# Kernel optimization log

Measured on AMD Instinct MI355X. Metric: run time of the kernel, lower is better.

Reference implementation:

```python
import jax, jax.numpy as jnp
import numpy as np
from jax.scipy.special import digamma, gammaln

B, N, H, W, D = 16, 1024, 32, 32, 256
TEMP = 0.5
KL_WEIGHT = 1e-3


def setup_inputs() -> dict:
    key = jax.random.key(0)
    k1, k2, k3 = jax.random.split(key, 3)
    logits = jax.random.normal(k1, (B, N, H, W), dtype=jnp.float32)
    # codebook initialized uniform(-1/N, 1/N) as in init_type == 'uniform'
    codebook = jax.random.uniform(k2, (N, D), dtype=jnp.float32,
                                  minval=-1.0 / N, maxval=1.0 / N)
    # uniform noise for the Gumbel-softmax rsample (channels-last layout [B,H,W,N])
    uniform_noise = jax.random.uniform(k3, (B, H, W, N), dtype=jnp.float32,
                                       minval=1e-6, maxval=1.0 - 1e-6)
    return {"logits": logits, "codebook": codebook, "uniform_noise": uniform_noise}


def reference(logits, codebook, uniform_noise):
    # convert_to_alpha: evidential mapping alpha = softplus(logits) + 1,
    # then permute(0,2,3,1) -> [B, H, W, N]
    alpha = jax.nn.softplus(jnp.transpose(logits, (0, 2, 3, 1))) + 1.0
    S = jnp.sum(alpha, axis=-1, keepdims=True)            # [B,H,W,1]
    probs = alpha / S                                      # [B,H,W,N]

    # RelaxedOneHotCategorical(temp, probs).rsample() == Gumbel-softmax
    gumbel = -jnp.log(-jnp.log(uniform_noise))
    sample = jax.nn.softmax((jnp.log(probs) + gumbel) / TEMP, axis=-1)  # [B,H,W,N]

    vector_weights = jnp.transpose(sample, (0, 3, 1, 2))   # [B,N,H,W]
    indices = jnp.argmax(vector_weights, axis=1)           # [B,H,W]

    # quantized output via codebook combine
    z_q = jnp.einsum('bnhw,nd->bdhw', vector_weights, codebook)  # [B,D,H,W]

    # KL( Dirichlet(alpha) || Dirichlet(ones(N)) ), closed form with beta=1:
    # lgamma(S) - sum lgamma(alpha) - lgamma(N) + sum (alpha-1)*(digamma(alpha)-digamma(S))
    S1 = S[..., 0]
    kl = (gammaln(S1)
          - jnp.sum(gammaln(alpha), axis=-1)
          - gammaln(jnp.float32(N))
          + jnp.sum((alpha - 1.0) * (digamma(alpha) - digamma(S)), axis=-1))
    kl_loss = KL_WEIGHT * jnp.mean(kl)

    # perplexity over soft encodings
    avg_probs = jnp.mean(sample.reshape(-1, N), axis=0)
    perplexity = jnp.exp(-jnp.sum(avg_probs * jnp.log(avg_probs + 1e-10)))

    return (z_q, kl_loss, indices, perplexity)
```

## Files before the change

### kernel.cpp

```cpp
#include <hip/hip_runtime.h>
#include <math.h>

#define NB 16
#define NN 1024
#define NH 32
#define NW 32
#define ND 256
#define NPIX (NB*NH*NW)

#define ZQ_OFF  0
#define KL_OFF  4194304
#define IDX_OFF 4194305
#define PPL_OFF 4210689

#define LGAMMA_1024F 6071.2804f
#define BS_ROW_B 2080

typedef _Float16 f16x8 __attribute__((ext_vector_type(8)));
typedef _Float16 f16x4 __attribute__((ext_vector_type(4)));
typedef float    f32x4 __attribute__((ext_vector_type(4)));

__device__ __forceinline__ float fast_rcp(float x){ return __builtin_amdgcn_rcpf(x); }

__device__ __forceinline__ void lgamma_digamma(float a, float& lg, float& dg){
    float a1 = a + 1.f, a2 = a + 2.f, a3 = a + 3.f, z = a + 4.f;
    float p01 = a*a1, p23 = a2*a3;
    float prod = p01*p23;
    float rz = fast_rcp(z);
    float rp = fast_rcp(prod);
    float lz = __logf(z);
    float lp = __logf(prod);
    float rz2 = rz*rz;
    lg = (z - 0.5f)*lz - z + 0.918938533f
       + rz*(0.083333333f - 0.002777778f*rz2) - lp;
    float sr = ((a + a + 1.f)*p23 + (a + a + 5.f)*p01)*rp;
    dg = lz - 0.5f*rz - rz2*(0.083333333f - 0.008333333f*rz2) - sr;
}

__device__ __forceinline__ float elem(float x, float u,
                                      float& S, float& L, float& P){
    float t  = __expf(-fabsf(x));
    float a  = fmaxf(x, 0.f) + __logf(1.f + t) + 1.f;
    float lg, dg;
    lgamma_digamma(a, lg, dg);
    S += a; L += lg; P += (a - 1.f)*dg;
    float d = 1.f - u;
    float lup = -d*(1.f + d*(0.5f + d*(0.33333333f + d*(0.25f
              + d*(0.2f + d*(0.16666667f + d*0.14285714f))))));
    float lu = (d < 0.09f) ? lup : __logf(u);
    float ar = a * fast_rcp(lu);
    return ar*ar;
}

__global__ __launch_bounds__(256) void k_tr(
    const float* __restrict__ cb, _Float16* __restrict__ cbT)
{
    const int kb = blockIdx.x, kq = blockIdx.y, d = threadIdx.x;
    _Float16 tmp[8];
#pragma unroll
    for (int i = 0; i < 8; ++i)
        tmp[i] = (_Float16)cb[(size_t)(32*kb + 8*kq + i)*ND + d];
    *(f16x8*)(cbT + (size_t)kb*8192 + (size_t)d*32 + 8*kq) = *(f16x8*)tmp;
}

__global__ __launch_bounds__(512, 4) void k_mega(
    const float* __restrict__ logits, const float* __restrict__ noise,
    const _Float16* __restrict__ cbT, float* __restrict__ colpart,
    float* __restrict__ klpart, float* __restrict__ out)
{
    __shared__ __align__(16) char lds[16*BS_ROW_B + 6*128*4];
    char*  bsb  = lds;
    float* redS = (float*)(lds + 16*BS_ROW_B);
    float* redL = redS + 128;
    float* redP = redL + 128;
    float* redZ = redP + 128;
    float* redM = redZ + 128;
    int*   redI = (int*)(redM + 128);

    const int t    = threadIdx.x;
    const int row  = blockIdx.x >> 1;
    const int w0   = (blockIdx.x & 1) * 16;
    const int b    = row >> 5, h = row & 31;
    const int lane = t & 63;
    const int v    = t >> 6;
    const int wl   = lane & 15;
    const int j4   = lane >> 4;
    const int p    = row*32 + w0 + wl;
    const int nq   = 4*v + j4;

    const float* lgB = logits + (size_t)b*(NN*NH*NW) + (size_t)(4*nq)*(NH*NW)
                     + (size_t)h*NW + w0 + wl;
    const float* nzB = noise  + (size_t)p*NN + 4*nq;

    float4 u4[8];
    float  xs[8][4];
    float  ev[32];
    float S = 0.f, L = 0.f, P = 0.f, Z = 0.f;
    float mx = -1.f;
    int   idx = 0;

#define CHUNK_LOAD(kk) do{                                        \
    u4[kk] = *(const float4*)(nzB + 128*(kk));                    \
    xs[kk][0] = lgB[(size_t)(128*(kk)+0)*(NH*NW)];                \
    xs[kk][1] = lgB[(size_t)(128*(kk)+1)*(NH*NW)];                \
    xs[kk][2] = lgB[(size_t)(128*(kk)+2)*(NH*NW)];                \
    xs[kk][3] = lgB[(size_t)(128*(kk)+3)*(NH*NW)]; }while(0)

#define DO_E(kk,mm,UC) do{                                        \
    float e = elem(xs[kk][mm], UC, S, L, P);                      \
    Z += e;                                                       \
    if (e > mx){ mx = e; idx = 128*(kk) + 4*nq + (mm); }          \
    ev[4*(kk)+(mm)] = e; }while(0)

    CHUNK_LOAD(0); CHUNK_LOAD(1); CHUNK_LOAD(2);
#pragma unroll
    for (int k = 0; k < 8; ++k){
        if (k < 5) CHUNK_LOAD(k+3);
        DO_E(k,0,u4[k].x);
        DO_E(k,1,u4[k].y);
        DO_E(k,2,u4[k].z);
        DO_E(k,3,u4[k].w);
    }
#undef CHUNK_LOAD
#undef DO_E

#pragma unroll
    for (int mask = 16; mask < 64; mask <<= 1){
        S += __shfl_xor(S, mask);
        L += __shfl_xor(L, mask);
        P += __shfl_xor(P, mask);
        Z += __shfl_xor(Z, mask);
        float mo = __shfl_xor(mx, mask);
        int   io = __shfl_xor(idx, mask);
        bool take = (mo > mx) || (mo == mx && io < idx);
        mx  = take ? mo : mx;
        idx = take ? io : idx;
    }
    if (j4 == 0){
        redS[16*v + wl] = S;  redL[16*v + wl] = L;
        redP[16*v + wl] = P;  redZ[16*v + wl] = Z;
        redM[16*v + wl] = mx; redI[16*v + wl] = idx;
    }
    __syncthreads();

    float Zt = 0.f;
#pragma unroll
    for (int qz = 0; qz < 8; ++qz) Zt += redZ[16*qz + wl];
    const float zinv = fast_rcp(Zt);

    {
        char* brow = bsb + wl*BS_ROW_B;
        const int sw   = wl & 7;
        const int sub8 = (nq & 1) << 3;
        const int cb2  = nq >> 1;
#pragma unroll
        for (int k = 0; k < 8; ++k){
            f16x4 hv;
            hv[0] = (_Float16)(ev[4*k+0]*zinv);
            hv[1] = (_Float16)(ev[4*k+1]*zinv);
            hv[2] = (_Float16)(ev[4*k+2]*zinv);
            hv[3] = (_Float16)(ev[4*k+3]*zinv);
            *(f16x4*)(brow + (((16*k + cb2) ^ sw) << 4) + sub8) = hv;
        }
    }

    if (t < 16){
        float Sa = 0.f, La = 0.f, Pa = 0.f, M = -1.f;
        int I = 0x7fffffff;
#pragma unroll
        for (int qz = 0; qz < 8; ++qz){
            Sa += redS[16*qz + t]; La += redL[16*qz + t]; Pa += redP[16*qz + t];
            float m = redM[16*qz + t]; int i = redI[16*qz + t];
            bool take = (m > M) || (m == M && i < I);
            M = take ? m : M; I = take ? i : I;
        }
        out[IDX_OFF + row*32 + w0 + t] = (float)I;
        float rS  = fast_rcp(Sa);
        float lnS = __logf(Sa);
        float lgS = (Sa - 0.5f)*lnS - Sa + 0.918938533f + 0.083333333f*rS;
        float dgS = lnS - 0.5f*rS;
        float kl = lgS - La - LGAMMA_1024F + (Pa - dgS*(Sa - 1024.f));
#pragma unroll
        for (int mask = 1; mask < 16; mask <<= 1) kl += __shfl_xor(kl, mask);
        if (t == 0) klpart[blockIdx.x] = kl;
    }
    __syncthreads();

    const _Float16* aBase = cbT + (size_t)(32*v + wl)*32 + j4*8;
    const char* bRow = bsb + wl*BS_ROW_B;
    const int fsw = wl & 7;

    f32x4 acc0 = (f32x4)0.f, acc1 = (f32x4)0.f;
    f16x8 a0[3], a1[3];
    a0[0] = *(const f16x8*)(aBase);
    a1[0] = *(const f16x8*)(aBase + 512);
    a0[1] = *(const f16x8*)(aBase + 8192);
    a1[1] = *(const f16x8*)(aBase + 8192 + 512);

#pragma unroll
    for (int kb = 0; kb < 32; ++kb){
        if (kb + 2 < 32){
            a0[(kb+2)%3] = *(const f16x8*)(aBase + (size_t)(kb+2)*8192);
            a1[(kb+2)%3] = *(const f16x8*)(aBase + (size_t)(kb+2)*8192 + 512);
        }
        f16x8 bf = *(const f16x8*)(bRow + ((((kb << 2) | j4) ^ fsw) << 4));
        acc0 = __builtin_amdgcn_mfma_f32_16x16x32_f16(a0[kb%3], bf, acc0, 0, 0, 0);
        acc1 = __builtin_amdgcn_mfma_f32_16x16x32_f16(a1[kb%3], bf, acc1, 0, 0, 0);
    }

    float* outp = out + (size_t)b*(ND*1024) + h*32 + w0;
#pragma unroll
    for (int r = 0; r < 4; ++r){
        int d = 32*v + 4*j4 + r;
        outp[(size_t)d*1024 + wl]        = acc0[r];
        outp[(size_t)(d + 16)*1024 + wl] = acc1[r];
    }

    {
        float s0 = 0.f, s1 = 0.f;
        const int c0 = t, c1 = t + 512;
#pragma unroll
        for (int r = 0; r < 16; ++r){
            const char* br = bsb + r*BS_ROW_B;
            const int sw2 = r & 7;
            s0 += (float)*(const _Float16*)(br + ((((c0 >> 3) ^ sw2) << 4) + 2*(c0 & 7)));
            s1 += (float)*(const _Float16*)(br + ((((c1 >> 3) ^ sw2) << 4) + 2*(c1 & 7)));
        }
        float* cp = colpart + (size_t)blockIdx.x*NN;
        cp[c0] = s0;
        cp[c1] = s1;
    }
}

__global__ __launch_bounds__(256) void k_red(
    const float* __restrict__ colpart, float* __restrict__ colsum)
{
    __shared__ float red[8][32];
    const int nl = threadIdx.x & 31;
    const int rs = threadIdx.x >> 5;
    const int n  = blockIdx.x*32 + nl;
    const float* cp = colpart + (size_t)rs*128*NN + n;
    float s = 0.f;
#pragma unroll 8
    for (int r = 0; r < 128; ++r)
        s += cp[(size_t)r*NN];
    red[rs][nl] = s;
    __syncthreads();
    if (threadIdx.x < 32){
        float tot = 0.f;
#pragma unroll
        for (int i = 0; i < 8; ++i) tot += red[i][threadIdx.x];
        colsum[blockIdx.x*32 + threadIdx.x] = tot;
    }
}

__global__ __launch_bounds__(256) void k_final(
    const float* __restrict__ colsum, const float* __restrict__ klpart,
    float* __restrict__ out)
{
    __shared__ float red[8];
    const int tid = threadIdx.x;
    float s = 0.f, kls = 0.f;
#pragma unroll
    for (int n = tid; n < NN; n += 256){
        float avg = colsum[n] * (1.f/16384.f);
        s += avg * logf(avg + 1e-10f);
        kls += klpart[n];
    }
#pragma unroll
    for (int mask = 1; mask < 64; mask <<= 1){
        s   += __shfl_xor(s, mask);
        kls += __shfl_xor(kls, mask);
    }
    if ((tid & 63) == 0){ red[tid >> 6] = s; red[4 + (tid >> 6)] = kls; }
    __syncthreads();
    if (tid == 0){
        float tot = red[0] + red[1] + red[2] + red[3];
        float klt = red[4] + red[5] + red[6] + red[7];
        out[PPL_OFF] = expf(-tot);
        out[KL_OFF]  = 1e-3f * (klt * (1.f/16384.f));
    }
}

extern "C" void kernel_launch(void* const* d_in, const int* in_sizes, int n_in,
                              void* d_out, int out_size, void* d_ws, size_t ws_size,
                              hipStream_t stream)
{
    const float* logits = (const float*)d_in[0];
    const float* cb     = (const float*)d_in[1];
    const float* noise  = (const float*)d_in[2];
    float* out = (float*)d_out;

    float* colpart = (float*)d_ws;
    float* colsum  = colpart + (size_t)1024*NN;
    float* klpart  = colsum + NN;
    _Float16* cbT  = (_Float16*)(klpart + NN);

    k_tr   <<<dim3(32, 4), 256, 0, stream>>>(cb, cbT);
    k_mega <<<dim3(1024),  512, 0, stream>>>(logits, noise, cbT, colpart, klpart, out);
    k_red  <<<dim3(32),    256, 0, stream>>>(colpart, colsum);
    k_final<<<1, 256, 0, stream>>>(colsum, klpart, out);
}
```

Baseline: 211.7 us.

## Double block to 1024 threads, halve per-thread work, shorten lgamma shift

The fused kernel now runs 1024 threads per block, so each thread processes 16 codebook entries instead of 32 and each wave computes one 16-wide MFMA output tile instead of two. The intent is more latency hiding and lower register pressure per thread. The lgamma/digamma recurrence shift drops from 4 to 3 terms, which saves arithmetic but may lose some accuracy for small alpha. Scheduling barriers pin the load prefetch order, and the KL reduction is moved after the matmul.

```diff
diff --git a/kernel.cpp b/kernel.cpp
--- a/kernel.cpp
+++ b/kernel.cpp
@@ -23,9 +23,9 @@
 __device__ __forceinline__ float fast_rcp(float x){ return __builtin_amdgcn_rcpf(x); }
 
 __device__ __forceinline__ void lgamma_digamma(float a, float& lg, float& dg){
-    float a1 = a + 1.f, a2 = a + 2.f, a3 = a + 3.f, z = a + 4.f;
-    float p01 = a*a1, p23 = a2*a3;
-    float prod = p01*p23;
+    float a1 = a + 1.f, a2 = a + 2.f, z = a + 3.f;
+    float t12  = a1*a2;
+    float prod = a*t12;
     float rz = fast_rcp(z);
     float rp = fast_rcp(prod);
     float lz = __logf(z);
@@ -33,7 +33,7 @@
     float rz2 = rz*rz;
     lg = (z - 0.5f)*lz - z + 0.918938533f
        + rz*(0.083333333f - 0.002777778f*rz2) - lp;
-    float sr = ((a + a + 1.f)*p23 + (a + a + 5.f)*p01)*rp;
+    float sr = (t12 + a*(a + a + 3.f))*rp;
     dg = lz - 0.5f*rz - rz2*(0.083333333f - 0.008333333f*rz2) - sr;
 }
 
@@ -63,19 +63,19 @@
     *(f16x8*)(cbT + (size_t)kb*8192 + (size_t)d*32 + 8*kq) = *(f16x8*)tmp;
 }
 
-__global__ __launch_bounds__(512, 4) void k_mega(
+__global__ __launch_bounds__(1024, 4) void k_mega(
     const float* __restrict__ logits, const float* __restrict__ noise,
     const _Float16* __restrict__ cbT, float* __restrict__ colpart,
     float* __restrict__ klpart, float* __restrict__ out)
 {
-    __shared__ __align__(16) char lds[16*BS_ROW_B + 6*128*4];
+    __shared__ __align__(16) char lds[16*BS_ROW_B + 6*256*4];
     char*  bsb  = lds;
     float* redS = (float*)(lds + 16*BS_ROW_B);
-    float* redL = redS + 128;
-    float* redP = redL + 128;
-    float* redZ = redP + 128;
-    float* redM = redZ + 128;
-    int*   redI = (int*)(redM + 128);
+    float* redL = redS + 256;
+    float* redP = redL + 256;
+    float* redZ = redP + 256;
+    float* redM = redZ + 256;
+    int*   redI = (int*)(redM + 256);
 
     const int t    = threadIdx.x;
     const int row  = blockIdx.x >> 1;
@@ -84,7 +84,7 @@
     const int lane = t & 63;
     const int v    = t >> 6;
     const int wl   = lane & 15;
-    const int j4   = lane >> 4;
+    const int j4   = (lane >> 4) & 3;
     const int p    = row*32 + w0 + wl;
     const int nq   = 4*v + j4;
 
@@ -92,30 +92,31 @@
                      + (size_t)h*NW + w0 + wl;
     const float* nzB = noise  + (size_t)p*NN + 4*nq;
 
-    float4 u4[8];
-    float  xs[8][4];
-    float  ev[32];
+    float4 u4[4];
+    float  xs[4][4];
+    float  ev[16];
     float S = 0.f, L = 0.f, P = 0.f, Z = 0.f;
     float mx = -1.f;
     int   idx = 0;
 
 #define CHUNK_LOAD(kk) do{                                        \
-    u4[kk] = *(const float4*)(nzB + 128*(kk));                    \
-    xs[kk][0] = lgB[(size_t)(128*(kk)+0)*(NH*NW)];                \
-    xs[kk][1] = lgB[(size_t)(128*(kk)+1)*(NH*NW)];                \
-    xs[kk][2] = lgB[(size_t)(128*(kk)+2)*(NH*NW)];                \
-    xs[kk][3] = lgB[(size_t)(128*(kk)+3)*(NH*NW)]; }while(0)
+    u4[kk] = *(const float4*)(nzB + 256*(kk));                    \
+    xs[kk][0] = lgB[(size_t)(256*(kk)+0)*(NH*NW)];                \
+    xs[kk][1] = lgB[(size_t)(256*(kk)+1)*(NH*NW)];                \
+    xs[kk][2] = lgB[(size_t)(256*(kk)+2)*(NH*NW)];                \
+    xs[kk][3] = lgB[(size_t)(256*(kk)+3)*(NH*NW)]; }while(0)
 
 #define DO_E(kk,mm,UC) do{                                        \
     float e = elem(xs[kk][mm], UC, S, L, P);                      \
     Z += e;                                                       \
-    if (e > mx){ mx = e; idx = 128*(kk) + 4*nq + (mm); }          \
+    if (e > mx){ mx = e; idx = 256*(kk) + 4*nq + (mm); }          \
     ev[4*(kk)+(mm)] = e; }while(0)
 
-    CHUNK_LOAD(0); CHUNK_LOAD(1); CHUNK_LOAD(2);
-#pragma unroll
-    for (int k = 0; k < 8; ++k){
-        if (k < 5) CHUNK_LOAD(k+3);
+    CHUNK_LOAD(0); CHUNK_LOAD(1);
+    __builtin_amdgcn_sched_barrier(0);
+#pragma unroll
+    for (int k = 0; k < 4; ++k){
+        if (k < 2){ CHUNK_LOAD(k+2); __builtin_amdgcn_sched_barrier(0); }
         DO_E(k,0,u4[k].x);
         DO_E(k,1,u4[k].y);
         DO_E(k,2,u4[k].z);
@@ -145,7 +146,7 @@
 
     float Zt = 0.f;
 #pragma unroll
-    for (int qz = 0; qz < 8; ++qz) Zt += redZ[16*qz + wl];
+    for (int qz = 0; qz < 16; ++qz) Zt += redZ[16*qz + wl];
     const float zinv = fast_rcp(Zt);
 
     {
@@ -154,21 +155,61 @@
         const int sub8 = (nq & 1) << 3;
         const int cb2  = nq >> 1;
 #pragma unroll
-        for (int k = 0; k < 8; ++k){
+        for (int k = 0; k < 4; ++k){
             f16x4 hv;
             hv[0] = (_Float16)(ev[4*k+0]*zinv);
             hv[1] = (_Float16)(ev[4*k+1]*zinv);
             hv[2] = (_Float16)(ev[4*k+2]*zinv);
             hv[3] = (_Float16)(ev[4*k+3]*zinv);
-            *(f16x4*)(brow + (((16*k + cb2) ^ sw) << 4) + sub8) = hv;
-        }
+            *(f16x4*)(brow + (((32*k + cb2) ^ sw) << 4) + sub8) = hv;
+        }
+    }
+    __syncthreads();
+
+    const _Float16* aBase = cbT + (size_t)(16*v + wl)*32 + j4*8;
+    const char* bRow = bsb + wl*BS_ROW_B;
+    const int fsw = wl & 7;
+
+    f32x4 acc = (f32x4)0.f;
+    f16x8 ar[4];
+    ar[0] = *(const f16x8*)(aBase);
+    ar[1] = *(const f16x8*)(aBase + 8192);
+    ar[2] = *(const f16x8*)(aBase + 2*8192);
+    __builtin_amdgcn_sched_barrier(0);
+
+#pragma unroll
+    for (int kb = 0; kb < 32; ++kb){
+        if (kb + 3 < 32){
+            ar[(kb+3)&3] = *(const f16x8*)(aBase + (size_t)(kb+3)*8192);
+            __builtin_amdgcn_sched_barrier(0);
+        }
+        f16x8 bf = *(const f16x8*)(bRow + ((((kb << 2) | j4) ^ fsw) << 4));
+        acc = __builtin_amdgcn_mfma_f32_16x16x32_f16(ar[kb&3], bf, acc, 0, 0, 0);
+    }
+
+    float* outp = out + (size_t)b*(ND*1024) + h*32 + w0;
+#pragma unroll
+    for (int r = 0; r < 4; ++r){
+        int d = 16*v + 4*j4 + r;
+        outp[(size_t)d*1024 + wl] = acc[r];
+    }
+
+    {
+        float s0 = 0.f;
+#pragma unroll
+        for (int r = 0; r < 16; ++r){
+            const char* br = bsb + r*BS_ROW_B;
+            const int sw2 = r & 7;
+            s0 += (float)*(const _Float16*)(br + ((((t >> 3) ^ sw2) << 4) + 2*(t & 7)));
+        }
+        colpart[(size_t)blockIdx.x*NN + t] = s0;
     }
 
     if (t < 16){
         float Sa = 0.f, La = 0.f, Pa = 0.f, M = -1.f;
         int I = 0x7fffffff;
 #pragma unroll
-        for (int qz = 0; qz < 8; ++qz){
+        for (int qz = 0; qz < 16; ++qz){
             Sa += redS[16*qz + t]; La += redL[16*qz + t]; Pa += redP[16*qz + t];
             float m = redM[16*qz + t]; int i = redI[16*qz + t];
             bool take = (m > M) || (m == M && i < I);
@@ -183,52 +224,6 @@
 #pragma unroll
         for (int mask = 1; mask < 16; mask <<= 1) kl += __shfl_xor(kl, mask);
         if (t == 0) klpart[blockIdx.x] = kl;
-    }
-    __syncthreads();
-
-    const _Float16* aBase = cbT + (size_t)(32*v + wl)*32 + j4*8;
-    const char* bRow = bsb + wl*BS_ROW_B;
-    const int fsw = wl & 7;
-
-    f32x4 acc0 = (f32x4)0.f, acc1 = (f32x4)0.f;
-    f16x8 a0[3], a1[3];
-    a0[0] = *(const f16x8*)(aBase);
-    a1[0] = *(const f16x8*)(aBase + 512);
-    a0[1] = *(const f16x8*)(aBase + 8192);
-    a1[1] = *(const f16x8*)(aBase + 8192 + 512);
-
-#pragma unroll
-    for (int kb = 0; kb < 32; ++kb){
-        if (kb + 2 < 32){
-            a0[(kb+2)%3] = *(const f16x8*)(aBase + (size_t)(kb+2)*8192);
-            a1[(kb+2)%3] = *(const f16x8*)(aBase + (size_t)(kb+2)*8192 + 512);
-        }
-        f16x8 bf = *(const f16x8*)(bRow + ((((kb << 2) | j4) ^ fsw) << 4));
-        acc0 = __builtin_amdgcn_mfma_f32_16x16x32_f16(a0[kb%3], bf, acc0, 0, 0, 0);
-        acc1 = __builtin_amdgcn_mfma_f32_16x16x32_f16(a1[kb%3], bf, acc1, 0, 0, 0);
-    }
-
-    float* outp = out + (size_t)b*(ND*1024) + h*32 + w0;
-#pragma unroll
-    for (int r = 0; r < 4; ++r){
-        int d = 32*v + 4*j4 + r;
-        outp[(size_t)d*1024 + wl]        = acc0[r];
-        outp[(size_t)(d + 16)*1024 + wl] = acc1[r];
-    }
-
-    {
-        float s0 = 0.f, s1 = 0.f;
-        const int c0 = t, c1 = t + 512;
-#pragma unroll
-        for (int r = 0; r < 16; ++r){
-            const char* br = bsb + r*BS_ROW_B;
-            const int sw2 = r & 7;
-            s0 += (float)*(const _Float16*)(br + ((((c0 >> 3) ^ sw2) << 4) + 2*(c0 & 7)));
-            s1 += (float)*(const _Float16*)(br + ((((c1 >> 3) ^ sw2) << 4) + 2*(c1 & 7)));
-        }
-        float* cp = colpart + (size_t)blockIdx.x*NN;
-        cp[c0] = s0;
-        cp[c1] = s1;
     }
 }
 
@@ -297,7 +292,7 @@
     _Float16* cbT  = (_Float16*)(klpart + NN);
 
     k_tr   <<<dim3(32, 4), 256, 0, stream>>>(cb, cbT);
-    k_mega <<<dim3(1024),  512, 0, stream>>>(logits, noise, cbT, colpart, klpart, out);
+    k_mega <<<dim3(1024), 1024, 0, stream>>>(logits, noise, cbT, colpart, klpart, out);
     k_red  <<<dim3(32),    256, 0, stream>>>(colpart, colsum);
     k_final<<<1, 256, 0, stream>>>(colsum, klpart, out);
 }
```

Result: faster. 205.9 us (-2.7%).
